# Kernel optimization log

Measured on AMD Instinct MI355X. Metric: run time of the kernel, lower is better.

Reference implementation:

```python
import jax, jax.numpy as jnp
import numpy as np

N_NODES = 100000
N_EDGES = 640000
F_IN = 128
HID = 128
N_CLS = 40


def _glorot(key, fan_in, fan_out):
    lim = float(np.sqrt(6.0 / (fan_in + fan_out)))
    return jax.random.uniform(key, (fan_in, fan_out), jnp.float32, -lim, lim)


def setup_inputs() -> dict:
    key = jax.random.key(0)
    ks = jax.random.split(key, 10)
    x = jax.random.normal(ks[0], (N_NODES, F_IN), jnp.float32)
    edge_index = jax.random.randint(ks[1], (2, N_EDGES), 0, N_NODES, jnp.int64 if jax.config.jax_enable_x64 else jnp.int32)
    W1 = _glorot(ks[2], F_IN, HID)
    W2 = _glorot(ks[3], HID, HID)
    W3 = _glorot(ks[4], HID, HID)
    W4 = _glorot(ks[5], HID, N_CLS)
    b1 = jnp.zeros((HID,), jnp.float32)
    b2 = jnp.zeros((HID,), jnp.float32)
    b3 = jnp.zeros((HID,), jnp.float32)
    b4 = jnp.zeros((N_CLS,), jnp.float32)
    return {"x": x, "edge_index": edge_index,
            "W1": W1, "b1": b1, "W2": W2, "b2": b2,
            "W3": W3, "b3": b3, "W4": W4, "b4": b4}


def _prep_edges(edge_index, n):
    # add self-loops, compute symmetric normalization deg^{-1/2}[src]*deg^{-1/2}[dst]
    loop = jnp.arange(n, dtype=edge_index.dtype)
    src = jnp.concatenate([edge_index[0], loop])
    dst = jnp.concatenate([edge_index[1], loop])
    deg = jax.ops.segment_sum(jnp.ones_like(dst, jnp.float32), dst, num_segments=n)
    dinv = jnp.where(deg > 0, jax.lax.rsqrt(deg), 0.0)
    norm = dinv[src] * dinv[dst]  # [E + n]
    return src, dst, norm


def _gcn_conv(x, W, b, src, dst, norm, n):
    h = x @ W                      # dense linear transform [n, out]
    msg = h[src] * norm[:, None]   # gather + scale over edges
    out = jax.ops.segment_sum(msg, dst, num_segments=n)  # scatter-add
    return out + b


def reference(x, edge_index, W1, b1, W2, b2, W3, b3, W4, b4):
    n = x.shape[0]
    src, dst, norm = _prep_edges(edge_index, n)
    h = jax.nn.relu(_gcn_conv(x, W1, b1, src, dst, norm, n))
    h = jax.nn.relu(_gcn_conv(h, W2, b2, src, dst, norm, n))
    h = jax.nn.relu(_gcn_conv(h, W3, b3, src, dst, norm, n))
    h = _gcn_conv(h, W4, b4, src, dst, norm, n)
    return jax.nn.log_softmax(h, axis=1)
```

## Files before the change

### kernel.cpp

```cpp
#include <hip/hip_runtime.h>
#include <math.h>

#define N_NODES 100000
#define N_EDGES 640000

typedef __bf16 bf16x8 __attribute__((ext_vector_type(8)));
typedef float f32x4 __attribute__((ext_vector_type(4)));

__device__ __forceinline__ unsigned short f2b(float x) {
  unsigned int u = __float_as_uint(x);
  u = (u + 0x7FFFu + ((u >> 16) & 1u)) >> 16;
  return (unsigned short)u;
}
__device__ __forceinline__ float blo(unsigned int v) { return __uint_as_float(v << 16); }
__device__ __forceinline__ float bhi(unsigned int v) { return __uint_as_float(v & 0xFFFF0000u); }

__device__ __forceinline__ int fragidx(int nn, int k) {
  int ct = nn >> 4, m = nn & 15;
  int kc = k >> 5, q = (k >> 3) & 3, e = k & 7;
  return (((ct * 4 + kc) * 4 + q) * 16 + m) * 8 + e;
}


__global__ __launch_bounds__(256) void k_count(const int* __restrict__ dst, int* __restrict__ deg, int e) {
  int i = blockIdx.x * 256 + threadIdx.x;
  if (i < e) atomicAdd(&deg[dst[i]], 1);
}

__global__ __launch_bounds__(256) void k_alloc(const int* __restrict__ deg, int* __restrict__ row_ptr,
                                               int* __restrict__ fillpos, int* __restrict__ col,
                                               float* __restrict__ dinv, int* __restrict__ counter, int n) {
  __shared__ int sdata[256];
  __shared__ int sbase;
  int tid = threadIdx.x;
  int i = blockIdx.x * 256 + tid;
  int d = (i < n) ? deg[i] : 0;
  sdata[tid] = d;
  __syncthreads();
  for (int off = 1; off < 256; off <<= 1) {
    int v = (tid >= off) ? sdata[tid - off] : 0;
    __syncthreads();
    sdata[tid] += v;
    __syncthreads();
  }
  if (tid == 255) sbase = atomicAdd(counter, sdata[255]);
  __syncthreads();
  int base = sbase;
  if (i < n) {
    int rp = base + sdata[tid] - d;
    row_ptr[i] = rp;
    fillpos[i] = rp + 1;
    col[rp] = i;
    dinv[i] = rsqrtf((float)d);
  }
}

__global__ __launch_bounds__(256) void k_fill(const int* __restrict__ src, const int* __restrict__ dst,
                                              int* __restrict__ fillpos, int* __restrict__ col, int e) {
  int i = blockIdx.x * 256 + threadIdx.x;
  if (i < e) {
    int d = dst[i];
    int p = atomicAdd(&fillpos[d], 1);
    col[p] = src[i];
  }
}


__global__ __launch_bounds__(256) void k_prep0(const float* __restrict__ W1, const float* __restrict__ W2,
                                               const float* __restrict__ W3, const float* __restrict__ W4,
                                               unsigned short* __restrict__ Wt, unsigned short* __restrict__ Wt4,
                                               unsigned short* __restrict__ Ha, unsigned short* __restrict__ Hc,
                                               unsigned short* __restrict__ H4,
                                               int* __restrict__ deg, int* __restrict__ counter, int n) {
  int b = blockIdx.x;
  int tid = threadIdx.x;
  if (b < 391) {
    int i = b * 256 + tid;
    if (i < n) deg[i] = 1;
    if (i == 0) *counter = 0;
  } else if (b < 583) {
    int bb = b - 391;
    const float* W = (bb < 64) ? W1 : (bb < 128) ? W2 : W3;
    unsigned short* D = Wt + ((bb < 64) ? 0 : (bb < 128) ? 16384 : 32768);
    int idx = (bb & 63) * 256 + tid;
    int k = idx >> 7, nn = idx & 127;
    D[fragidx(nn, k)] = f2b(W[idx]);
  } else if (b < 607) {
    int idx = (b - 583) * 256 + tid;
    int nn = idx >> 7, k = idx & 127;
    Wt4[fragidx(nn, k)] = (nn < 40) ? f2b(W4[(size_t)k * 40 + nn]) : (unsigned short)0;
  } else if (b == 607) {
    if (tid < 128) Ha[(size_t)n * 128 + tid] = 0;
    else Hc[(size_t)n * 128 + (tid - 128)] = 0;
  } else {
    if (tid < 48) H4[(size_t)n * 40 + tid] = 0;
  }
}

#define SXP 136


__global__ __launch_bounds__(256) void k_gemm1(const float* __restrict__ X,
                                               const unsigned short* __restrict__ Wt,
                                               const float* __restrict__ dinv,
                                               unsigned short* __restrict__ H, int n) {
  int tid = threadIdx.x;
  int row0 = blockIdx.x * 64;
  int wave = tid >> 6, lane = tid & 63;
  int m = lane & 15, q = lane >> 4;
  int grow = row0 + wave * 16 + m;
  if (grow >= n) grow = n - 1;
  const float4* X4 = (const float4*)X;
  uint4 a4[4];
#pragma unroll
  for (int kc = 0; kc < 4; ++kc) {
    float4 f0 = X4[(size_t)grow * 32 + kc * 8 + q * 2];
    float4 f1 = X4[(size_t)grow * 32 + kc * 8 + q * 2 + 1];
    a4[kc].x = (unsigned int)f2b(f0.x) | ((unsigned int)f2b(f0.y) << 16);
    a4[kc].y = (unsigned int)f2b(f0.z) | ((unsigned int)f2b(f0.w) << 16);
    a4[kc].z = (unsigned int)f2b(f1.x) | ((unsigned int)f2b(f1.y) << 16);
    a4[kc].w = (unsigned int)f2b(f1.z) | ((unsigned int)f2b(f1.w) << 16);
  }
  const bf16x8* Wf = (const bf16x8*)Wt;
  f32x4 acc[8];
#pragma unroll
  for (int ct = 0; ct < 8; ++ct) acc[ct] = (f32x4){0.f, 0.f, 0.f, 0.f};
#pragma unroll
  for (int kc = 0; kc < 4; ++kc) {
    bf16x8 a = *(bf16x8*)&a4[kc];
#pragma unroll
    for (int ct = 0; ct < 8; ++ct) {
      bf16x8 b = Wf[(ct * 4 + kc) * 64 + lane];
      acc[ct] = __builtin_amdgcn_mfma_f32_16x16x32_bf16(a, b, acc[ct], 0, 0, 0);
    }
  }
#pragma unroll
  for (int r = 0; r < 4; ++r) {
    int row = row0 + wave * 16 + q * 4 + r;
    if (row < n) {
      float di = dinv[row];
#pragma unroll
      for (int ct = 0; ct < 8; ++ct)
        H[(size_t)row * 128 + ct * 16 + m] = f2b(acc[ct][r] * di);
    }
  }
}


template <int NCT>
__global__ __launch_bounds__(256) void k_fag(const unsigned short* __restrict__ Hin,
                                             const int* __restrict__ col,
                                             const int* __restrict__ row_ptr,
                                             const int* __restrict__ deg,
                                             const float* __restrict__ dinv,
                                             const float* __restrict__ bias,
                                             const unsigned short* __restrict__ Wt,
                                             unsigned short* __restrict__ Hout, int n) {
  __shared__ unsigned short sW[NCT * 2048];
  __shared__ unsigned short sX[64 * SXP];
  int tid = threadIdx.x;
  int row0 = blockIdx.x * 64;
  int ql = tid & 15;
  int qbase = tid & 48;
  const uint4* Hg = (const uint4*)Hin;
  int starts[4], cnts[4], mycs[4];
  float dinvs[4];
#pragma unroll
  for (int it = 0; it < 4; ++it) {
    int node = row0 + (tid >> 4) + (it << 4);
    int nc = (node < n) ? node : 0;
    starts[it] = row_ptr[nc];
    cnts[it] = deg[nc];
    dinvs[it] = dinv[nc];
  }
#pragma unroll
  for (int it = 0; it < 4; ++it) {
    int c0 = (cnts[it] < 15) ? cnts[it] : 15;
    mycs[it] = (ql < c0) ? col[starts[it] + ql] : n;
  }
  uint4 v[4][8];
#pragma unroll
  for (int it = 0; it < 4; ++it) {
#pragma unroll
    for (int jj = 0; jj < 8; ++jj) {
      int c = __shfl(mycs[it], qbase + jj, 64);
      v[it][jj] = Hg[(size_t)c * 16 + ql];
    }
  }
  {
    const uint4* W4 = (const uint4*)Wt;
    uint4* sW4 = (uint4*)sW;
#pragma unroll
    for (int i = 0; i < NCT; ++i) sW4[i * 256 + tid] = W4[i * 256 + tid];
  }
  float4 b0 = ((const float4*)bias)[ql * 2];
  float4 b1 = ((const float4*)bias)[ql * 2 + 1];
#pragma unroll
  for (int it = 0; it < 4; ++it) {
    int node = row0 + (tid >> 4) + (it << 4);
    int cnt = cnts[it];
    int cnt0 = (cnt < 15) ? cnt : 15;
    int myc = mycs[it];
    bool r2 = (cnt0 > 8);
    uint4 w2[8];
    if (r2) {
#pragma unroll
      for (int jj = 0; jj < 8; ++jj) {
        int c = __shfl(myc, qbase + 8 + jj, 64);
        w2[jj] = Hg[(size_t)c * 16 + ql];
      }
    }
    float s0 = 0.f, s1 = 0.f, s2 = 0.f, s3 = 0.f, s4 = 0.f, s5 = 0.f, s6 = 0.f, s7 = 0.f;
#pragma unroll
    for (int jj = 0; jj < 8; ++jj) {
      s0 += blo(v[it][jj].x); s1 += bhi(v[it][jj].x);
      s2 += blo(v[it][jj].y); s3 += bhi(v[it][jj].y);
      s4 += blo(v[it][jj].z); s5 += bhi(v[it][jj].z);
      s6 += blo(v[it][jj].w); s7 += bhi(v[it][jj].w);
    }
    if (r2) {
#pragma unroll
      for (int jj = 0; jj < 8; ++jj) {
        s0 += blo(w2[jj].x); s1 += bhi(w2[jj].x);
        s2 += blo(w2[jj].y); s3 += bhi(w2[jj].y);
        s4 += blo(w2[jj].z); s5 += bhi(w2[jj].z);
        s6 += blo(w2[jj].w); s7 += bhi(w2[jj].w);
      }
    }
    for (int j = 15; j < cnt; ++j) {
      int c = col[starts[it] + j];
      uint4 t = Hg[(size_t)c * 16 + ql];
      s0 += blo(t.x); s1 += bhi(t.x);
      s2 += blo(t.y); s3 += bhi(t.y);
      s4 += blo(t.z); s5 += bhi(t.z);
      s6 += blo(t.w); s7 += bhi(t.w);
    }
    if (node < n) {
      float di = dinvs[it];
      float o0 = fmaf(s0, di, b0.x), o1 = fmaf(s1, di, b0.y);
      float o2 = fmaf(s2, di, b0.z), o3 = fmaf(s3, di, b0.w);
      float o4 = fmaf(s4, di, b1.x), o5 = fmaf(s5, di, b1.y);
      float o6 = fmaf(s6, di, b1.z), o7 = fmaf(s7, di, b1.w);
      o0 = o0 > 0.f ? o0 : 0.f; o1 = o1 > 0.f ? o1 : 0.f;
      o2 = o2 > 0.f ? o2 : 0.f; o3 = o3 > 0.f ? o3 : 0.f;
      o4 = o4 > 0.f ? o4 : 0.f; o5 = o5 > 0.f ? o5 : 0.f;
      o6 = o6 > 0.f ? o6 : 0.f; o7 = o7 > 0.f ? o7 : 0.f;
      uint4 w;
      w.x = (unsigned int)f2b(o0) | ((unsigned int)f2b(o1) << 16);
      w.y = (unsigned int)f2b(o2) | ((unsigned int)f2b(o3) << 16);
      w.z = (unsigned int)f2b(o4) | ((unsigned int)f2b(o5) << 16);
      w.w = (unsigned int)f2b(o6) | ((unsigned int)f2b(o7) << 16);
      *(uint4*)&sX[(node - row0) * SXP + ql * 8] = w;
    }
  }
  __syncthreads();
  int wave = tid >> 6, lane = tid & 63;
  int m = lane & 15, q = lane >> 4;
  int grow = row0 + wave * 16 + m;
  if (grow >= n) grow = n - 1;
  int lrow = grow - row0;
  uint4 a4[4];
#pragma unroll
  for (int kc = 0; kc < 4; ++kc) a4[kc] = *(const uint4*)&sX[lrow * SXP + kc * 32 + q * 8];
  const bf16x8* Wl = (const bf16x8*)sW;
  f32x4 acc[NCT];
#pragma unroll
  for (int ct = 0; ct < NCT; ++ct) acc[ct] = (f32x4){0.f, 0.f, 0.f, 0.f};
#pragma unroll
  for (int kc = 0; kc < 4; ++kc) {
    bf16x8 a = *(bf16x8*)&a4[kc];
#pragma unroll
    for (int ct = 0; ct < NCT; ++ct) {
      bf16x8 b = Wl[(ct * 4 + kc) * 64 + lane];
      acc[ct] = __builtin_amdgcn_mfma_f32_16x16x32_bf16(a, b, acc[ct], 0, 0, 0);
    }
  }
#pragma unroll
  for (int r = 0; r < 4; ++r) {
    int row = row0 + wave * 16 + q * 4 + r;
    if (row < n) {
      float di = dinv[row];
      if constexpr (NCT == 8) {
#pragma unroll
        for (int ct = 0; ct < 8; ++ct)
          Hout[(size_t)row * 128 + ct * 16 + m] = f2b(acc[ct][r] * di);
      } else {
#pragma unroll
        for (int ct = 0; ct < NCT; ++ct) {
          int c = ct * 16 + m;
          if (c < 40) Hout[(size_t)row * 40 + c] = f2b(acc[ct][r] * di);
        }
      }
    }
  }
}


__global__ __launch_bounds__(256) void k_agg40_lsm(const unsigned short* __restrict__ H, const int* __restrict__ col,
                                                   const int* __restrict__ row_ptr, const int* __restrict__ deg,
                                                   const float* __restrict__ dinv, const float* __restrict__ bias,
                                                   float* __restrict__ out, int n) {
  int node = blockIdx.x * 4 + (threadIdx.x >> 6);
  int lane = threadIdx.x & 63;
  if (node >= n) return;
  const unsigned int* H1 = (const unsigned int*)H;
  int start = row_ptr[node];
  int cnt = deg[node];
  int cnt0 = (cnt < 63) ? cnt : 63;
  int myc = (lane < cnt0) ? col[start + lane] : n;
  int slice = (lane >= 20) + (lane >= 40);
  int pr = lane - slice * 20;
  pr = (pr > 19) ? 19 : pr;
  int rounds = (cnt0 + 2) / 3;
  float ax = 0.f, ay = 0.f;
  for (int rb = 0; rb < rounds; rb += 4) {
    unsigned int v[4];
#pragma unroll
    for (int j = 0; j < 4; ++j) {
      int idx = (rb + j) * 3 + slice;
      idx = (idx > 63) ? 63 : idx;
      int c = __shfl(myc, idx, 64);
      v[j] = H1[(size_t)c * 20 + pr];
    }
#pragma unroll
    for (int j = 0; j < 4; ++j) { ax += blo(v[j]); ay += bhi(v[j]); }
  }
  if (lane < 20) {
    for (int j = 63; j < cnt; ++j) {
      int c = col[start + j];
      unsigned int v = H1[(size_t)c * 20 + pr];
      ax += blo(v);
      ay += bhi(v);
    }
  }
  float ax1 = __shfl(ax, lane + 20, 64), ay1 = __shfl(ay, lane + 20, 64);
  float ax2 = __shfl(ax, lane + 40, 64), ay2 = __shfl(ay, lane + 40, 64);
  float di = dinv[node];
  float2 b2 = ((const float2*)bias)[pr];
  float c0 = fmaf(ax + ax1 + ax2, di, b2.x);
  float c1 = fmaf(ay + ay1 + ay2, di, b2.y);
  float v = (lane < 20) ? fmaxf(c0, c1) : -INFINITY;
#pragma unroll
  for (int off = 32; off > 0; off >>= 1) v = fmaxf(v, __shfl_xor(v, off, 64));
  float e = (lane < 20) ? (__expf(c0 - v) + __expf(c1 - v)) : 0.f;
#pragma unroll
  for (int off = 32; off > 0; off >>= 1) e += __shfl_xor(e, off, 64);
  if (lane < 20) {
    float ls = v + __logf(e);
    ((float2*)out)[(size_t)node * 20 + lane] = make_float2(c0 - ls, c1 - ls);
  }
}


extern "C" void kernel_launch(void* const* d_in, const int* in_sizes, int n_in,
                              void* d_out, int out_size, void* d_ws, size_t ws_size,
                              hipStream_t stream) {
  const float* x  = (const float*)d_in[0];
  const int* edge = (const int*)d_in[1];
  const float* W1 = (const float*)d_in[2];
  const float* b1 = (const float*)d_in[3];
  const float* W2 = (const float*)d_in[4];
  const float* b2 = (const float*)d_in[5];
  const float* W3 = (const float*)d_in[6];
  const float* b3 = (const float*)d_in[7];
  const float* W4 = (const float*)d_in[8];
  const float* b4 = (const float*)d_in[9];
  float* out = (float*)d_out;

  const int n = N_NODES, E = N_EDGES;
  const int* srcp = edge;
  const int* dstp = edge + E;

  char* ws = (char*)d_ws;
  size_t off = 0;
  auto alloc = [&](size_t bytes) -> void* {
    void* p = ws + off;
    off = (off + bytes + 255) & ~(size_t)255;
    return p;
  };
  int*   deg     = (int*)alloc((size_t)n * 4);
  int*   row_ptr = (int*)alloc((size_t)n * 4);
  int*   fillpos = (int*)alloc((size_t)n * 4);
  float* dinv    = (float*)alloc((size_t)n * 4);
  int*   counter = (int*)alloc(256);
  int*   colx    = (int*)alloc((size_t)(E + n) * 4);
  unsigned short* Ha  = (unsigned short*)alloc((size_t)(n + 1) * 128 * 2);
  unsigned short* Hc  = (unsigned short*)alloc((size_t)(n + 1) * 128 * 2);
  unsigned short* H4  = (unsigned short*)alloc(((size_t)(n + 1) * 40 + 16) * 2);
  unsigned short* Wt  = (unsigned short*)alloc((size_t)3 * 128 * 128 * 2);
  unsigned short* Wt4 = (unsigned short*)alloc((size_t)48 * 128 * 2);
  (void)ws_size; (void)in_sizes; (void)n_in; (void)out_size;

  k_prep0<<<609, 256, 0, stream>>>(W1, W2, W3, W4, Wt, Wt4, Ha, Hc, H4, deg, counter, n);
  k_count<<<(E + 255) / 256, 256, 0, stream>>>(dstp, deg, E);
  k_alloc<<<(n + 255) / 256, 256, 0, stream>>>(deg, row_ptr, fillpos, colx, dinv, counter, n);
  k_fill <<<(E + 255) / 256, 256, 0, stream>>>(srcp, dstp, fillpos, colx, E);

  const int gg = (n + 63) / 64, ga = (n + 3) / 4;
  k_gemm1<<<gg, 256, 0, stream>>>(x, Wt, dinv, Ha, n);
  k_fag<8><<<gg, 256, 0, stream>>>(Ha, colx, row_ptr, deg, dinv, b1, Wt + 16384, Hc, n);
  k_fag<8><<<gg, 256, 0, stream>>>(Hc, colx, row_ptr, deg, dinv, b2, Wt + 32768, Ha, n);
  k_fag<3><<<gg, 256, 0, stream>>>(Ha, colx, row_ptr, deg, dinv, b3, Wt4, H4, n);
  k_agg40_lsm<<<ga, 256, 0, stream>>>(H4, colx, row_ptr, deg, dinv, b4, out, n);
}
```

Measured before the change: 341.3 us.

## Split hidden features into two 64-column planes for gather-aggregation locality

Stores the 128-wide bf16 hidden activations as two separate 64-column planes, each of (n+1) rows. The aggregation gathers one plane at a time, so each 128-byte neighbor row is served by 8 lanes. Pairs of lanes split the neighbor list and combine partial sums with an xor shuffle. The weight copy into shared memory is moved to the start of the kernel. The goal is better cache locality for the random gathers, since each pass touches only half the feature matrix. The cost is extra shuffles and two passes over the neighbor indices.

```diff
diff --git a/kernel.cpp b/kernel.cpp
--- a/kernel.cpp
+++ b/kernel.cpp
@@ -20,6 +20,7 @@
   int kc = k >> 5, q = (k >> 3) & 3, e = k & 7;
   return (((ct * 4 + kc) * 4 + q) * 16 + m) * 8 + e;
 }
+
 
 
 __global__ __launch_bounds__(256) void k_count(const int* __restrict__ dst, int* __restrict__ deg, int e) {
@@ -90,8 +91,12 @@
     int nn = idx >> 7, k = idx & 127;
     Wt4[fragidx(nn, k)] = (nn < 40) ? f2b(W4[(size_t)k * 40 + nn]) : (unsigned short)0;
   } else if (b == 607) {
-    if (tid < 128) Ha[(size_t)n * 128 + tid] = 0;
-    else Hc[(size_t)n * 128 + (tid - 128)] = 0;
+    size_t RS = (size_t)(n + 1) * 64;
+    int which = tid >> 7;
+    int r = (tid >> 6) & 1;
+    int o = tid & 63;
+    unsigned short* P = which ? Hc : Ha;
+    P[r * RS + (size_t)n * 64 + o] = 0;
   } else {
     if (tid < 48) H4[(size_t)n * 40 + tid] = 0;
   }
@@ -134,6 +139,7 @@
       acc[ct] = __builtin_amdgcn_mfma_f32_16x16x32_bf16(a, b, acc[ct], 0, 0, 0);
     }
   }
+  size_t RS = (size_t)(n + 1) * 64;
 #pragma unroll
   for (int r = 0; r < 4; ++r) {
     int row = row0 + wave * 16 + q * 4 + r;
@@ -141,7 +147,7 @@
       float di = dinv[row];
 #pragma unroll
       for (int ct = 0; ct < 8; ++ct)
-        H[(size_t)row * 128 + ct * 16 + m] = f2b(acc[ct][r] * di);
+        H[(ct >> 2) * RS + (size_t)row * 64 + (ct & 3) * 16 + m] = f2b(acc[ct][r] * di);
     }
   }
 }
@@ -160,9 +166,17 @@
   __shared__ unsigned short sX[64 * SXP];
   int tid = threadIdx.x;
   int row0 = blockIdx.x * 64;
+  {
+    const uint4* W4 = (const uint4*)Wt;
+    uint4* sW4 = (uint4*)sW;
+#pragma unroll
+    for (int i = 0; i < NCT; ++i) sW4[i * 256 + tid] = W4[i * 256 + tid];
+  }
   int ql = tid & 15;
   int qbase = tid & 48;
-  const uint4* Hg = (const uint4*)Hin;
+  int sub = ql >> 3;
+  int chunk = ql & 7;
+  const size_t RS = (size_t)(n + 1) * 64;
   int starts[4], cnts[4], mycs[4];
   float dinvs[4];
 #pragma unroll
@@ -178,69 +192,62 @@
     int c0 = (cnts[it] < 15) ? cnts[it] : 15;
     mycs[it] = (ql < c0) ? col[starts[it] + ql] : n;
   }
-  uint4 v[4][8];
-#pragma unroll
-  for (int it = 0; it < 4; ++it) {
-#pragma unroll
-    for (int jj = 0; jj < 8; ++jj) {
-      int c = __shfl(mycs[it], qbase + jj, 64);
-      v[it][jj] = Hg[(size_t)c * 16 + ql];
+  float acc8[4][8];
+#pragma unroll
+  for (int r = 0; r < 2; ++r) {
+    const uint4* Hr = (const uint4*)(Hin + r * RS);
+#pragma unroll
+    for (int it = 0; it < 4; ++it) {
+      uint4 v[8];
+#pragma unroll
+      for (int t = 0; t < 8; ++t) {
+        int jj = sub + 2 * t;
+        int c = __shfl(mycs[it], qbase + jj, 64);
+        v[t] = Hr[(size_t)c * 8 + chunk];
+      }
+      float s0 = 0.f, s1 = 0.f, s2 = 0.f, s3 = 0.f, s4 = 0.f, s5 = 0.f, s6 = 0.f, s7 = 0.f;
+#pragma unroll
+      for (int t = 0; t < 8; ++t) {
+        s0 += blo(v[t].x); s1 += bhi(v[t].x);
+        s2 += blo(v[t].y); s3 += bhi(v[t].y);
+        s4 += blo(v[t].z); s5 += bhi(v[t].z);
+        s6 += blo(v[t].w); s7 += bhi(v[t].w);
+      }
+      s0 += __shfl_xor(s0, 8, 64); s1 += __shfl_xor(s1, 8, 64);
+      s2 += __shfl_xor(s2, 8, 64); s3 += __shfl_xor(s3, 8, 64);
+      s4 += __shfl_xor(s4, 8, 64); s5 += __shfl_xor(s5, 8, 64);
+      s6 += __shfl_xor(s6, 8, 64); s7 += __shfl_xor(s7, 8, 64);
+      if (sub == r) {
+        acc8[it][0] = s0; acc8[it][1] = s1; acc8[it][2] = s2; acc8[it][3] = s3;
+        acc8[it][4] = s4; acc8[it][5] = s5; acc8[it][6] = s6; acc8[it][7] = s7;
+      }
     }
   }
   {
-    const uint4* W4 = (const uint4*)Wt;
-    uint4* sW4 = (uint4*)sW;
-#pragma unroll
-    for (int i = 0; i < NCT; ++i) sW4[i * 256 + tid] = W4[i * 256 + tid];
+    const uint4* Hm = (const uint4*)(Hin + sub * RS);
+#pragma unroll
+    for (int it = 0; it < 4; ++it) {
+      for (int j = 15; j < cnts[it]; ++j) {
+        int c = col[starts[it] + j];
+        uint4 t4 = Hm[(size_t)c * 8 + chunk];
+        acc8[it][0] += blo(t4.x); acc8[it][1] += bhi(t4.x);
+        acc8[it][2] += blo(t4.y); acc8[it][3] += bhi(t4.y);
+        acc8[it][4] += blo(t4.z); acc8[it][5] += bhi(t4.z);
+        acc8[it][6] += blo(t4.w); acc8[it][7] += bhi(t4.w);
+      }
+    }
   }
   float4 b0 = ((const float4*)bias)[ql * 2];
   float4 b1 = ((const float4*)bias)[ql * 2 + 1];
 #pragma unroll
   for (int it = 0; it < 4; ++it) {
     int node = row0 + (tid >> 4) + (it << 4);
-    int cnt = cnts[it];
-    int cnt0 = (cnt < 15) ? cnt : 15;
-    int myc = mycs[it];
-    bool r2 = (cnt0 > 8);
-    uint4 w2[8];
-    if (r2) {
-#pragma unroll
-      for (int jj = 0; jj < 8; ++jj) {
-        int c = __shfl(myc, qbase + 8 + jj, 64);
-        w2[jj] = Hg[(size_t)c * 16 + ql];
-      }
-    }
-    float s0 = 0.f, s1 = 0.f, s2 = 0.f, s3 = 0.f, s4 = 0.f, s5 = 0.f, s6 = 0.f, s7 = 0.f;
-#pragma unroll
-    for (int jj = 0; jj < 8; ++jj) {
-      s0 += blo(v[it][jj].x); s1 += bhi(v[it][jj].x);
-      s2 += blo(v[it][jj].y); s3 += bhi(v[it][jj].y);
-      s4 += blo(v[it][jj].z); s5 += bhi(v[it][jj].z);
-      s6 += blo(v[it][jj].w); s7 += bhi(v[it][jj].w);
-    }
-    if (r2) {
-#pragma unroll
-      for (int jj = 0; jj < 8; ++jj) {
-        s0 += blo(w2[jj].x); s1 += bhi(w2[jj].x);
-        s2 += blo(w2[jj].y); s3 += bhi(w2[jj].y);
-        s4 += blo(w2[jj].z); s5 += bhi(w2[jj].z);
-        s6 += blo(w2[jj].w); s7 += bhi(w2[jj].w);
-      }
-    }
-    for (int j = 15; j < cnt; ++j) {
-      int c = col[starts[it] + j];
-      uint4 t = Hg[(size_t)c * 16 + ql];
-      s0 += blo(t.x); s1 += bhi(t.x);
-      s2 += blo(t.y); s3 += bhi(t.y);
-      s4 += blo(t.z); s5 += bhi(t.z);
-      s6 += blo(t.w); s7 += bhi(t.w);
-    }
     if (node < n) {
       float di = dinvs[it];
-      float o0 = fmaf(s0, di, b0.x), o1 = fmaf(s1, di, b0.y);
-      float o2 = fmaf(s2, di, b0.z), o3 = fmaf(s3, di, b0.w);
-      float o4 = fmaf(s4, di, b1.x), o5 = fmaf(s5, di, b1.y);
-      float o6 = fmaf(s6, di, b1.z), o7 = fmaf(s7, di, b1.w);
+      float o0 = fmaf(acc8[it][0], di, b0.x), o1 = fmaf(acc8[it][1], di, b0.y);
+      float o2 = fmaf(acc8[it][2], di, b0.z), o3 = fmaf(acc8[it][3], di, b0.w);
+      float o4 = fmaf(acc8[it][4], di, b1.x), o5 = fmaf(acc8[it][5], di, b1.y);
+      float o6 = fmaf(acc8[it][6], di, b1.z), o7 = fmaf(acc8[it][7], di, b1.w);
       o0 = o0 > 0.f ? o0 : 0.f; o1 = o1 > 0.f ? o1 : 0.f;
       o2 = o2 > 0.f ? o2 : 0.f; o3 = o3 > 0.f ? o3 : 0.f;
       o4 = o4 > 0.f ? o4 : 0.f; o5 = o5 > 0.f ? o5 : 0.f;
@@ -281,9 +288,10 @@
     if (row < n) {
       float di = dinv[row];
       if constexpr (NCT == 8) {
+        size_t RSo = (size_t)(n + 1) * 64;
 #pragma unroll
         for (int ct = 0; ct < 8; ++ct)
-          Hout[(size_t)row * 128 + ct * 16 + m] = f2b(acc[ct][r] * di);
+          Hout[(ct >> 2) * RSo + (size_t)row * 64 + (ct & 3) * 16 + m] = f2b(acc[ct][r] * di);
       } else {
 #pragma unroll
         for (int ct = 0; ct < NCT; ++ct) {
```

Result: no change. 347.3 us (+1.8%).
